# Kernel optimization log

Hardware: AMD Instinct MI355X
Metric: run time of the kernel (lower is better)

Reference implementation:

```python
import math
import jax, jax.numpy as jnp
import numpy as np

BATCH, DEPTH = 16, 12
N_NODES = 2 ** DEPTH - 1  # 4095, heap layout: children of i are 2i+1, 2i+2
IN_F, OUT_F, STATE_F = 512, 512, 256


def setup_inputs() -> dict:
    key = jax.random.key(0)
    ks = jax.random.split(key, 10)
    x_batch = jax.random.normal(ks[0], (BATCH, N_NODES, IN_F), dtype=jnp.float32)
    idx_batch = jnp.arange(BATCH, dtype=jnp.int32)
    W_in = jax.random.normal(ks[1], (IN_F, IN_F), dtype=jnp.float32) / math.sqrt(IN_F)
    b_in = jnp.zeros((IN_F,), dtype=jnp.float32)
    u1 = jax.random.uniform(ks[2], (STATE_F,), dtype=jnp.float32)
    u2 = jax.random.uniform(ks[3], (STATE_F,), dtype=jnp.float32)
    nu_log = jnp.log(-0.5 * jnp.log(u1 + 1e-6))
    theta_log = jnp.log(2.0 * math.pi * u2)
    lam_mod = jnp.exp(-jnp.exp(nu_log))
    gamma_log = jnp.log(jnp.sqrt(1.0 - jnp.square(lam_mod)))
    B_re = jax.random.normal(ks[4], (STATE_F, IN_F), dtype=jnp.float32) / math.sqrt(2 * IN_F)
    B_im = jax.random.normal(ks[5], (STATE_F, IN_F), dtype=jnp.float32) / math.sqrt(2 * IN_F)
    C_re = jax.random.normal(ks[6], (OUT_F, STATE_F), dtype=jnp.float32) / math.sqrt(STATE_F)
    C_im = jax.random.normal(ks[7], (OUT_F, STATE_F), dtype=jnp.float32) / math.sqrt(STATE_F)
    return dict(x_batch=x_batch, idx_batch=idx_batch, W_in=W_in, b_in=b_in,
                nu_log=nu_log, theta_log=theta_log, gamma_log=gamma_log,
                B_re=B_re, B_im=B_im, C_re=C_re, C_im=C_im)


def reference(x_batch, idx_batch, W_in, b_in, nu_log, theta_log, gamma_log,
              B_re, B_im, C_re, C_im):
    bsz, n_nodes, _ = x_batch.shape
    depth = int(round(math.log2(n_nodes + 1)))
    S = B_re.shape[0]

    # LRU constants (complex lambda kept as (re, im) pair)
    lam_mod = jnp.exp(-jnp.exp(nu_log))           # [S]
    th = jnp.exp(theta_log)
    lr, li = lam_mod * jnp.cos(th), lam_mod * jnp.sin(th)
    gamma = jnp.exp(gamma_log)                    # [S]

    proj = x_batch @ W_in.T + b_in                # [B, N, IN]
    # complex input term (proj is real): proj @ B^T
    in_re = jnp.einsum('bni,si->bns', proj, B_re) # [B, N, S]
    in_im = jnp.einsum('bni,si->bns', proj, B_im)

    h_re = jnp.zeros((bsz, n_nodes, S), dtype=proj.dtype)
    h_im = jnp.zeros((bsz, n_nodes, S), dtype=proj.dtype)

    # process levels bottom-up; level d nodes occupy [2^d-1, 2^{d+1}-1)
    for d in range(depth - 1, -1, -1):
        a, b = 2 ** d - 1, 2 ** (d + 1) - 1
        n = b - a
        if d == depth - 1:  # leaves: left/right = -1 -> zero child state
            cr = jnp.zeros((bsz, n, S), dtype=proj.dtype)
            ci = jnp.zeros((bsz, n, S), dtype=proj.dtype)
        else:
            # children of nodes [a, b) are the contiguous block [2a+1, 2b+1)
            cr = h_re[:, 2 * a + 1:2 * b + 1].reshape(bsz, n, 2, S).sum(axis=2)
            ci = h_im[:, 2 * a + 1:2 * b + 1].reshape(bsz, n, 2, S).sum(axis=2)
        hr = lr * cr - li * ci + gamma * in_re[:, a:b]
        hi = lr * ci + li * cr + gamma * in_im[:, a:b]
        h_re = h_re.at[:, a:b].set(hr)
        h_im = h_im.at[:, a:b].set(hi)

    # y = Re(h @ C^T), computed once on final states (same math as per-level scatter)
    outputs = jnp.einsum('bns,os->bno', h_re, C_re) - jnp.einsum('bns,os->bno', h_im, C_im)
    return outputs
```

## Files before the change

### kernel.cpp

```cpp
#include <hip/hip_runtime.h>


#define ROWS 65520
#define KDIM 512

typedef __attribute__((ext_vector_type(8))) short bf16x8;
typedef __attribute__((ext_vector_type(4))) float f32x4;

__device__ __forceinline__ unsigned short f2bf(float f) {
    unsigned int u = __float_as_uint(f);
    unsigned int r = (u + 0x7FFFu + ((u >> 16) & 1u)) >> 16;
    return (unsigned short)r;
}
__device__ __forceinline__ float b2f(unsigned short h) {
    return __uint_as_float(((unsigned int)h) << 16);
}
__device__ __forceinline__ float b2f_lo(unsigned int p) {
    return __uint_as_float(p << 16);
}
__device__ __forceinline__ float b2f_hi(unsigned int p) {
    return __uint_as_float(p & 0xFFFF0000u);
}

#define PC_BASE   1024
#define PB_BASE   2048
#define CVT_BASE  2176
#define CVT_BLKS  2048
#define PREP_GRID 4224
#define CVT_N4    8386560
#define CVT_STR   (CVT_BLKS * 256)

__global__ __launch_bounds__(256) void prep_all(const float* __restrict__ x,
                                                unsigned short* __restrict__ x16,
                                                const float* __restrict__ W,
                                                const float* __restrict__ Bre,
                                                const float* __restrict__ Bim,
                                                const float* __restrict__ gamma_log,
                                                unsigned short* __restrict__ M16,
                                                const float* __restrict__ bin,
                                                float* __restrict__ biasc,
                                                const float* __restrict__ Cre,
                                                const float* __restrict__ Cim,
                                                unsigned short* __restrict__ C16) {
    __shared__ float Bs[16][17];
    __shared__ float Ws[16][17];
    const int blk = blockIdx.x;
    const int t = threadIdx.x;

    if (blk < PC_BASE) {
        const int bx = blk & 31;
        const int by = blk >> 5;
        const int tx = t & 15;
        const int ty = t >> 4;
        const int j  = bx * 16 + tx;
        const int cc = by * 16 + ty;
        const float* Bsel = (cc < 256) ? (Bre + (size_t)cc * 512)
                                       : (Bim + (size_t)(cc - 256) * 512);
        float acc = 0.f;
        for (int kt = 0; kt < 512; kt += 16) {
            Bs[ty][tx] = Bsel[kt + tx];
            Ws[ty][tx] = W[(size_t)(kt + ty) * 512 + j];
            __syncthreads();
#pragma unroll
            for (int k = 0; k < 16; ++k) acc += Bs[ty][k] * Ws[k][tx];
            __syncthreads();
        }
        float g = expf(gamma_log[cc & 255]);
        M16[(size_t)cc * 512 + j] = f2bf(acc * g);
    } else if (blk < PB_BASE) {
        int idx = (blk - PC_BASE) * 256 + t;
        int o = idx >> 9;
        int s = idx & 511;
        float v = (s < 256) ? Cre[(size_t)o * 256 + s] : -Cim[(size_t)o * 256 + (s - 256)];
        C16[idx] = f2bf(v);
    } else if (blk < CVT_BASE) {
        const int c = (blk - PB_BASE) * 4 + (t >> 6);
        const int lane = t & 63;
        const float* Bsel = (c < 256) ? (Bre + (size_t)c * 512)
                                      : (Bim + (size_t)(c - 256) * 512);
        float acc = 0.f;
#pragma unroll
        for (int i = lane; i < 512; i += 64) acc += bin[i] * Bsel[i];
#pragma unroll
        for (int off = 32; off > 0; off >>= 1) acc += __shfl_down(acc, off, 64);
        if (lane == 0) biasc[c] = acc * expf(gamma_log[c & 255]);
    } else {
        const int i = (blk - CVT_BASE) * 256 + t;
        const float4* src = (const float4*)x;
        ushort4* dst = (ushort4*)x16;
        if (i < CVT_N4 - 15 * CVT_STR) {
            float4 v0  = src[i];
            float4 v1  = src[i +  1 * CVT_STR];
            float4 v2  = src[i +  2 * CVT_STR];
            float4 v3  = src[i +  3 * CVT_STR];
            float4 v4  = src[i +  4 * CVT_STR];
            float4 v5  = src[i +  5 * CVT_STR];
            float4 v6  = src[i +  6 * CVT_STR];
            float4 v7  = src[i +  7 * CVT_STR];
            float4 v8  = src[i +  8 * CVT_STR];
            float4 v9  = src[i +  9 * CVT_STR];
            float4 v10 = src[i + 10 * CVT_STR];
            float4 v11 = src[i + 11 * CVT_STR];
            float4 v12 = src[i + 12 * CVT_STR];
            float4 v13 = src[i + 13 * CVT_STR];
            float4 v14 = src[i + 14 * CVT_STR];
            float4 v15 = src[i + 15 * CVT_STR];
#define CVT1(K, V)                                                             \
            { ushort4 o; o.x = f2bf(V.x); o.y = f2bf(V.y);                     \
              o.z = f2bf(V.z); o.w = f2bf(V.w); dst[i + (K) * CVT_STR] = o; }
            CVT1(0, v0)  CVT1(1, v1)  CVT1(2, v2)  CVT1(3, v3)
            CVT1(4, v4)  CVT1(5, v5)  CVT1(6, v6)  CVT1(7, v7)
            CVT1(8, v8)  CVT1(9, v9)  CVT1(10, v10) CVT1(11, v11)
            CVT1(12, v12) CVT1(13, v13) CVT1(14, v14) CVT1(15, v15)
#undef CVT1
        } else {
#pragma unroll
            for (int k = 0; k < 16; ++k) {
                int idx = i + k * CVT_STR;
                if (idx < CVT_N4) {
                    float4 v = src[idx];
                    ushort4 o;
                    o.x = f2bf(v.x); o.y = f2bf(v.y); o.z = f2bf(v.z); o.w = f2bf(v.w);
                    dst[idx] = o;
                }
            }
        }
    }
}

template <bool OUT_BF16>
__global__ __launch_bounds__(256) void gemm_mfma(const unsigned short* __restrict__ A,
                                                 const unsigned short* __restrict__ Bm,
                                                 const float* __restrict__ bias,
                                                 void* __restrict__ Cout,
                                                 int Mrows) {
    __shared__ __align__(16) unsigned short As[2][128 * 32];
    __shared__ __align__(16) unsigned short Bs[2][128 * 32];
    const int t = threadIdx.x;
    const int lane = t & 63;
    const int w = t >> 6;
    const int wr = (w >> 1) * 64;
    const int wc = (w & 1) * 64;
    const int p = blockIdx.x;
    const int xcd = p & 7;
    const int q = p >> 3;
    const int colblk = q & 3;
    const int rg = q >> 2;
    const int col0 = colblk * 128;

    int arow[2], akoff[2], ldsoff[2];
    const unsigned short* gbB[2];
#pragma unroll
    for (int qq = 0; qq < 2; ++qq) {
        int c_   = qq * 256 + t;
        int row_ = c_ >> 2;
        int sl_  = c_ & 3;
        int kc_  = (sl_ - (row_ >> 1)) & 3;
        arow[qq]  = row_;
        akoff[qq] = kc_ * 8;
        ldsoff[qq] = c_ * 8;
        gbB[qq] = Bm + (size_t)(col0 + row_) * KDIM + kc_ * 8;
    }
    const unsigned short* gaB[2];

#define SET_TILE_A(ROW0)                                                       \
    do {                                                                       \
        _Pragma("unroll")                                                      \
        for (int qq = 0; qq < 2; ++qq) {                                       \
            int ar_ = (ROW0) + arow[qq]; if (ar_ >= Mrows) ar_ = Mrows - 1;    \
            gaB[qq] = A + (size_t)ar_ * KDIM + akoff[qq];                      \
        }                                                                      \
    } while (0)

#define STAGE(pb, KT)                                                          \
    do {                                                                       \
        _Pragma("unroll")                                                      \
        for (int qq = 0; qq < 2; ++qq) {                                       \
            __builtin_amdgcn_global_load_lds(                                  \
                (const __attribute__((address_space(1))) unsigned int*)(gaB[qq] + (KT)), \
                (__attribute__((address_space(3))) unsigned int*)(&As[pb][ldsoff[qq]]), \
                16, 0, 0);                                                     \
            __builtin_amdgcn_global_load_lds(                                  \
                (const __attribute__((address_space(1))) unsigned int*)(gbB[qq] + (KT)), \
                (__attribute__((address_space(3))) unsigned int*)(&Bs[pb][ldsoff[qq]]), \
                16, 0, 0);                                                     \
        }                                                                      \
    } while (0)

    f32x4 acc[4][4] = {};

    int rowblk = xcd * 64 + rg * 4;
    int row0 = rowblk * 128;
    int kt0 = (rowblk & 15) * 32;
    SET_TILE_A(row0);
    STAGE(0, kt0);
    __syncthreads();

    int cur = 0;
    for (int j = 0; j < 4; ++j) {
        for (int it = 0; it < 16; ++it) {
            if (it < 15) {
                STAGE(cur ^ 1, (kt0 + (it + 1) * 32) & 511);
            } else if (j < 3) {
                const int nrowblk = rowblk + 1;
                SET_TILE_A(nrowblk * 128);
                STAGE(cur ^ 1, (nrowblk & 15) * 32);
            }
            __builtin_amdgcn_s_setprio(1);
            {
                bf16x8 af[4], bfr[4];
#pragma unroll
                for (int i = 0; i < 4; ++i) {
                    int row = wr + i * 16 + (lane & 15);
                    int sa  = ((lane >> 4) + (row >> 1)) & 3;
                    af[i] = *(const bf16x8*)(&As[cur][row * 32 + sa * 8]);
                    int colr = wc + i * 16 + (lane & 15);
                    int sb  = ((lane >> 4) + (colr >> 1)) & 3;
                    bfr[i] = *(const bf16x8*)(&Bs[cur][colr * 32 + sb * 8]);
                }
#pragma unroll
                for (int i = 0; i < 4; ++i)
#pragma unroll
                    for (int jj = 0; jj < 4; ++jj)
                        acc[i][jj] = __builtin_amdgcn_mfma_f32_16x16x32_bf16(
                            af[i], bfr[jj], acc[i][jj], 0, 0, 0);
            }
            __builtin_amdgcn_s_setprio(0);
            __syncthreads();
            cur ^= 1;
        }

        const int cq = lane >> 4;
        const int cl = lane & 15;
#pragma unroll
        for (int i = 0; i < 4; ++i) {
#pragma unroll
            for (int jj = 0; jj < 4; ++jj) {
#pragma unroll
                for (int r = 0; r < 4; ++r) {
                    int grow = row0 + wr + i * 16 + cq * 4 + r;
                    int gcol = col0 + wc + jj * 16 + cl;
                    if (grow < Mrows) {
                        float v = acc[i][jj][r];
                        if (bias) v += bias[gcol];
                        if (OUT_BF16)
                            ((unsigned short*)Cout)[(size_t)grow * 512 + gcol] = f2bf(v);
                        else
                            ((float*)Cout)[(size_t)grow * 512 + gcol] = v;
                    }
                    acc[i][jj][r] = 0.f;
                }
            }
        }

        rowblk += 1;
        row0 = rowblk * 128;
        kt0 = (rowblk & 15) * 32;
    }
#undef STAGE
#undef SET_TILE_A
}

template <int E>
__global__ __launch_bounds__(256) void tree_up2(unsigned short* __restrict__ buf,
                                                const float* __restrict__ nu_log,
                                                const float* __restrict__ theta_log,
                                                int root_base, int nroots) {
    const int b = blockIdx.x;
    const int h = threadIdx.x >> 7;
    const int j2 = (threadIdx.x & 127) * 2;
    const int rr = blockIdx.y * 2 + h;
    if (rr >= nroots) return;
    const int rs = root_base + rr;
    constexpr int LEAVES = 1 << E;
    constexpr int NODES = LEAVES - 1;

    float lr0, li0, lr1, li1;
    { const float lam = expf(-expf(nu_log[j2]));     const float th = expf(theta_log[j2]);
      lr0 = lam * cosf(th); li0 = lam * sinf(th); }
    { const float lam = expf(-expf(nu_log[j2 + 1])); const float th = expf(theta_log[j2 + 1]);
      lr1 = lam * cosf(th); li1 = lam * sinf(th); }
    const size_t base = (size_t)b * 4095;

    unsigned int pr[LEAVES], pi[LEAVES];
    const int nbL = ((rs + 1) << E) - 1;
#pragma unroll
    for (int i = 0; i < LEAVES; ++i) {
        const size_t r = (base + nbL + i) * 512;
        pr[i] = *(const unsigned int*)(buf + r + j2);
        pi[i] = *(const unsigned int*)(buf + r + 256 + j2);
    }
    unsigned int qr[NODES], qi[NODES];
#pragma unroll
    for (int e = E - 1; e >= 0; --e) {
#pragma unroll
        for (int i = 0; i < (1 << e); ++i) {
            const int idx = LEAVES - (2 << e) + i;
            const size_t r = (base + (((rs + 1) << e) - 1) + i) * 512;
            qr[idx] = *(const unsigned int*)(buf + r + j2);
            qi[idx] = *(const unsigned int*)(buf + r + 256 + j2);
        }
    }
    __builtin_amdgcn_sched_barrier(0);

    float vr0[LEAVES], vi0[LEAVES], vr1[LEAVES], vi1[LEAVES];
#pragma unroll
    for (int i = 0; i < LEAVES; ++i) {
        vr0[i] = b2f_lo(pr[i]); vr1[i] = b2f_hi(pr[i]);
        vi0[i] = b2f_lo(pi[i]); vi1[i] = b2f_hi(pi[i]);
    }
#pragma unroll
    for (int e = E - 1; e >= 0; --e) {
#pragma unroll
        for (int i = 0; i < (1 << e); ++i) {
            const int idx = LEAVES - (2 << e) + i;
            const float cr0 = vr0[2 * i] + vr0[2 * i + 1];
            const float ci0 = vi0[2 * i] + vi0[2 * i + 1];
            const float cr1 = vr1[2 * i] + vr1[2 * i + 1];
            const float ci1 = vi1[2 * i] + vi1[2 * i + 1];
            const float hr0 = lr0 * cr0 - li0 * ci0 + b2f_lo(qr[idx]);
            const float hi0 = lr0 * ci0 + li0 * cr0 + b2f_lo(qi[idx]);
            const float hr1 = lr1 * cr1 - li1 * ci1 + b2f_hi(qr[idx]);
            const float hi1 = lr1 * ci1 + li1 * cr1 + b2f_hi(qi[idx]);
            const size_t r = (base + (((rs + 1) << e) - 1) + i) * 512;
            *(unsigned int*)(buf + r + j2) =
                (unsigned int)f2bf(hr0) | ((unsigned int)f2bf(hr1) << 16);
            *(unsigned int*)(buf + r + 256 + j2) =
                (unsigned int)f2bf(hi0) | ((unsigned int)f2bf(hi1) << 16);
            vr0[i] = hr0; vi0[i] = hi0; vr1[i] = hr1; vi1[i] = hi1;
        }
    }
}

extern "C" void kernel_launch(void* const* d_in, const int* in_sizes, int n_in,
                              void* d_out, int out_size, void* d_ws, size_t ws_size,
                              hipStream_t stream) {
    const float* x         = (const float*)d_in[0];
    const float* W_in      = (const float*)d_in[2];
    const float* b_in      = (const float*)d_in[3];
    const float* nu_log    = (const float*)d_in[4];
    const float* theta_log = (const float*)d_in[5];
    const float* gamma_log = (const float*)d_in[6];
    const float* B_re      = (const float*)d_in[7];
    const float* B_im      = (const float*)d_in[8];
    const float* C_re      = (const float*)d_in[9];
    const float* C_im      = (const float*)d_in[10];
    float* out = (float*)d_out;

    char* ws = (char*)d_ws;
    const size_t HB = (size_t)ROWS * 512 * 2;
    unsigned short* x16   = (unsigned short*)ws;
    unsigned short* hb16  = (unsigned short*)(ws + HB);
    unsigned short* M16   = (unsigned short*)(ws + 2 * HB);
    unsigned short* C16   = (unsigned short*)(ws + 2 * HB + 512 * 512 * 2);
    float*          biasc = (float*)(ws + 2 * HB + 2 * 512 * 512 * 2);

    prep_all<<<PREP_GRID, 256, 0, stream>>>(x, x16, W_in, B_re, B_im, gamma_log,
                                            M16, b_in, biasc, C_re, C_im, C16);

    gemm_mfma<true><<<512, 256, 0, stream>>>(x16, M16, biasc, hb16, ROWS);

    tree_up2<4><<<dim3(16, 64), 256, 0, stream>>>(hb16, nu_log, theta_log, 127, 128);
    tree_up2<4><<<dim3(16, 4),  256, 0, stream>>>(hb16, nu_log, theta_log, 7, 8);
    tree_up2<3><<<dim3(16, 1),  256, 0, stream>>>(hb16, nu_log, theta_log, 0, 1);

    gemm_mfma<false><<<512, 256, 0, stream>>>(hb16, C16, nullptr, out, ROWS);
}
```

Measured before the change: 413.4 us.

## Retile GEMM to 256x256 blocks with 8 waves and split-phase staging

Each GEMM block now computes a 256x256 output tile with 512 threads (8 waves), replacing the 128x128 tile of 4 waves that looped over four row blocks. The K step grows to 64 with an XOR swizzle in LDS. Loads for the next stage are spread across four sub-phases separated by explicit s_barrier and vmcnt waits. The aim is more data reuse per byte loaded and better overlap of global-to-LDS copies with MFMA work, at the cost of 128KB of LDS, a large accumulator array (register pressure), and more barriers.

Result: no change. 406.8 us (-1.6%).

```diff
diff --git a/kernel.cpp b/kernel.cpp
--- a/kernel.cpp
+++ b/kernel.cpp
@@ -129,136 +129,146 @@
 }
 
 template <bool OUT_BF16>
-__global__ __launch_bounds__(256) void gemm_mfma(const unsigned short* __restrict__ A,
-                                                 const unsigned short* __restrict__ Bm,
-                                                 const float* __restrict__ bias,
-                                                 void* __restrict__ Cout,
-                                                 int Mrows) {
-    __shared__ __align__(16) unsigned short As[2][128 * 32];
-    __shared__ __align__(16) unsigned short Bs[2][128 * 32];
+__global__ __launch_bounds__(512, 2) void gemm_mfma(const unsigned short* __restrict__ A,
+                                                    const unsigned short* __restrict__ Bm,
+                                                    const float* __restrict__ bias,
+                                                    void* __restrict__ Cout,
+                                                    int Mrows) {
+    __shared__ __align__(16) unsigned short As[2][16384];
+    __shared__ __align__(16) unsigned short Bs[2][16384];
     const int t = threadIdx.x;
     const int lane = t & 63;
-    const int w = t >> 6;
-    const int wr = (w >> 1) * 64;
-    const int wc = (w & 1) * 64;
-    const int p = blockIdx.x;
-    const int xcd = p & 7;
-    const int q = p >> 3;
-    const int colblk = q & 3;
-    const int rg = q >> 2;
-    const int col0 = colblk * 128;
-
-    int arow[2], akoff[2], ldsoff[2];
-    const unsigned short* gbB[2];
-#pragma unroll
-    for (int qq = 0; qq < 2; ++qq) {
-        int c_   = qq * 256 + t;
-        int row_ = c_ >> 2;
-        int sl_  = c_ & 3;
-        int kc_  = (sl_ - (row_ >> 1)) & 3;
-        arow[qq]  = row_;
-        akoff[qq] = kc_ * 8;
-        ldsoff[qq] = c_ * 8;
-        gbB[qq] = Bm + (size_t)(col0 + row_) * KDIM + kc_ * 8;
-    }
-    const unsigned short* gaB[2];
-
-#define SET_TILE_A(ROW0)                                                       \
+    const int wn = t >> 6;
+    const int bid = blockIdx.x;
+    const int xcd = bid & 7;
+    const int lid = bid >> 3;
+    const int rt = xcd * 32 + (lid >> 1);
+    const int ct = lid & 1;
+    const int row0 = rt * 256;
+    const int col0 = ct * 256;
+
+    const unsigned short* gA[2][2];
+    const unsigned short* gB[2][2];
+#pragma unroll
+    for (int h = 0; h < 2; ++h) {
+#pragma unroll
+        for (int q = 0; q < 2; ++q) {
+            int c2  = q * 512 + t;
+            int row = c2 >> 3;
+            int kc  = c2 & 7;
+            int lrow = h * 128 + row;
+            int kg  = kc ^ (lrow & 7);
+            int ar  = row0 + lrow; if (ar >= Mrows) ar = Mrows - 1;
+            gA[h][q] = A + (size_t)ar * KDIM + kg * 8;
+            gB[h][q] = Bm + (size_t)(col0 + lrow) * KDIM + kg * 8;
+        }
+    }
+
+#define STG_A(BUF, H, KT)                                                      \
     do {                                                                       \
         _Pragma("unroll")                                                      \
-        for (int qq = 0; qq < 2; ++qq) {                                       \
-            int ar_ = (ROW0) + arow[qq]; if (ar_ >= Mrows) ar_ = Mrows - 1;    \
-            gaB[qq] = A + (size_t)ar_ * KDIM + akoff[qq];                      \
-        }                                                                      \
+        for (int q = 0; q < 2; ++q)                                            \
+            __builtin_amdgcn_global_load_lds(                                  \
+                (const __attribute__((address_space(1))) unsigned int*)(gA[H][q] + (KT)), \
+                (__attribute__((address_space(3))) unsigned int*)(&As[BUF][(H) * 8192 + (q * 512 + t) * 8]), \
+                16, 0, 0);                                                     \
     } while (0)
-
-#define STAGE(pb, KT)                                                          \
+#define STG_B(BUF, H, KT)                                                      \
     do {                                                                       \
         _Pragma("unroll")                                                      \
-        for (int qq = 0; qq < 2; ++qq) {                                       \
+        for (int q = 0; q < 2; ++q)                                            \
             __builtin_amdgcn_global_load_lds(                                  \
-                (const __attribute__((address_space(1))) unsigned int*)(gaB[qq] + (KT)), \
-                (__attribute__((address_space(3))) unsigned int*)(&As[pb][ldsoff[qq]]), \
+                (const __attribute__((address_space(1))) unsigned int*)(gB[H][q] + (KT)), \
+                (__attribute__((address_space(3))) unsigned int*)(&Bs[BUF][(H) * 8192 + (q * 512 + t) * 8]), \
                 16, 0, 0);                                                     \
-            __builtin_amdgcn_global_load_lds(                                  \
-                (const __attribute__((address_space(1))) unsigned int*)(gbB[qq] + (KT)), \
-                (__attribute__((address_space(3))) unsigned int*)(&Bs[pb][ldsoff[qq]]), \
-                16, 0, 0);                                                     \
-        }                                                                      \
     } while (0)
-
-    f32x4 acc[4][4] = {};
-
-    int rowblk = xcd * 64 + rg * 4;
-    int row0 = rowblk * 128;
-    int kt0 = (rowblk & 15) * 32;
-    SET_TILE_A(row0);
-    STAGE(0, kt0);
-    __syncthreads();
-
-    int cur = 0;
-    for (int j = 0; j < 4; ++j) {
-        for (int it = 0; it < 16; ++it) {
-            if (it < 15) {
-                STAGE(cur ^ 1, (kt0 + (it + 1) * 32) & 511);
-            } else if (j < 3) {
-                const int nrowblk = rowblk + 1;
-                SET_TILE_A(nrowblk * 128);
-                STAGE(cur ^ 1, (nrowblk & 15) * 32);
-            }
+#define BARRIER() asm volatile("s_barrier" ::: "memory")
+
+    f32x4 acc[16][2] = {};
+
+#define KTOF(S) ((((rt & 7) + (S)) & 7) * 64)
+
+    {
+        const int kt = KTOF(0);
+        STG_B(0, 0, kt); STG_B(0, 1, kt); STG_A(0, 0, kt); STG_A(0, 1, kt);
+    }
+
+    for (int s = 0; s < 8; ++s) {
+        const int cur = s & 1;
+        const int nkt = KTOF(s + 1);
+        asm volatile("s_waitcnt vmcnt(2)" ::: "memory");
+        BARRIER();
+#pragma unroll
+        for (int p = 0; p < 4; ++p) {
+            bf16x8 af[4][2], bfr[2][2];
+#pragma unroll
+            for (int i = 0; i < 4; ++i) {
+                int row = p * 64 + i * 16 + (lane & 15);
+#pragma unroll
+                for (int kk = 0; kk < 2; ++kk) {
+                    int kca = (kk * 4 + (lane >> 4)) ^ (row & 7);
+                    af[i][kk] = *(const bf16x8*)(&As[cur][row * 64 + kca * 8]);
+                }
+            }
+#pragma unroll
+            for (int j = 0; j < 2; ++j) {
+                int colr = wn * 32 + j * 16 + (lane & 15);
+#pragma unroll
+                for (int kk = 0; kk < 2; ++kk) {
+                    int kcb = (kk * 4 + (lane >> 4)) ^ (colr & 7);
+                    bfr[j][kk] = *(const bf16x8*)(&Bs[cur][colr * 64 + kcb * 8]);
+                }
+            }
+            if (s < 7) {
+                if (p == 0)      STG_B(cur ^ 1, 0, nkt);
+                else if (p == 1) STG_B(cur ^ 1, 1, nkt);
+                else if (p == 2) STG_A(cur ^ 1, 0, nkt);
+                else             STG_A(cur ^ 1, 1, nkt);
+            }
+            BARRIER();
             __builtin_amdgcn_s_setprio(1);
-            {
-                bf16x8 af[4], bfr[4];
-#pragma unroll
-                for (int i = 0; i < 4; ++i) {
-                    int row = wr + i * 16 + (lane & 15);
-                    int sa  = ((lane >> 4) + (row >> 1)) & 3;
-                    af[i] = *(const bf16x8*)(&As[cur][row * 32 + sa * 8]);
-                    int colr = wc + i * 16 + (lane & 15);
-                    int sb  = ((lane >> 4) + (colr >> 1)) & 3;
-                    bfr[i] = *(const bf16x8*)(&Bs[cur][colr * 32 + sb * 8]);
+#pragma unroll
+            for (int i = 0; i < 4; ++i)
+#pragma unroll
+                for (int j = 0; j < 2; ++j)
+#pragma unroll
+                    for (int kk = 0; kk < 2; ++kk)
+                        acc[p * 4 + i][j] = __builtin_amdgcn_mfma_f32_16x16x32_bf16(
+                            af[i][kk], bfr[j][kk], acc[p * 4 + i][j], 0, 0, 0);
+            __builtin_amdgcn_s_setprio(0);
+            if (p == 1) {
+                if (s < 7) asm volatile("s_waitcnt vmcnt(4)" ::: "memory");
+                else       asm volatile("s_waitcnt vmcnt(0)" ::: "memory");
+            }
+            BARRIER();
+        }
+    }
+#undef KTOF
+#undef BARRIER
+#undef STG_B
+#undef STG_A
+
+    const int cq = lane >> 4;
+    const int cl = lane & 15;
+#pragma unroll
+    for (int I = 0; I < 16; ++I) {
+#pragma unroll
+        for (int j = 0; j < 2; ++j) {
+#pragma unroll
+            for (int r = 0; r < 4; ++r) {
+                int grow = row0 + I * 16 + cq * 4 + r;
+                int gcol = col0 + wn * 32 + j * 16 + cl;
+                if (grow < Mrows) {
+                    float v = acc[I][j][r];
+                    if (bias) v += bias[gcol];
+                    if (OUT_BF16)
+                        ((unsigned short*)Cout)[(size_t)grow * 512 + gcol] = f2bf(v);
+                    else
+                        ((float*)Cout)[(size_t)grow * 512 + gcol] = v;
                 }
-#pragma unroll
-                for (int i = 0; i < 4; ++i)
-#pragma unroll
-                    for (int jj = 0; jj < 4; ++jj)
-                        acc[i][jj] = __builtin_amdgcn_mfma_f32_16x16x32_bf16(
-                            af[i], bfr[jj], acc[i][jj], 0, 0, 0);
-            }
-            __builtin_amdgcn_s_setprio(0);
-            __syncthreads();
-            cur ^= 1;
-        }
-
-        const int cq = lane >> 4;
-        const int cl = lane & 15;
-#pragma unroll
-        for (int i = 0; i < 4; ++i) {
-#pragma unroll
-            for (int jj = 0; jj < 4; ++jj) {
-#pragma unroll
-                for (int r = 0; r < 4; ++r) {
-                    int grow = row0 + wr + i * 16 + cq * 4 + r;
-                    int gcol = col0 + wc + jj * 16 + cl;
-                    if (grow < Mrows) {
-                        float v = acc[i][jj][r];
-                        if (bias) v += bias[gcol];
-                        if (OUT_BF16)
-                            ((unsigned short*)Cout)[(size_t)grow * 512 + gcol] = f2bf(v);
-                        else
-                            ((float*)Cout)[(size_t)grow * 512 + gcol] = v;
-                    }
-                    acc[i][jj][r] = 0.f;
-                }
-            }
-        }
-
-        rowblk += 1;
-        row0 = rowblk * 128;
-        kt0 = (rowblk & 15) * 32;
-    }
-#undef STAGE
-#undef SET_TILE_A
+            }
+        }
+    }
 }
 
 template <int E>
@@ -358,11 +368,11 @@
     prep_all<<<PREP_GRID, 256, 0, stream>>>(x, x16, W_in, B_re, B_im, gamma_log,
                                             M16, b_in, biasc, C_re, C_im, C16);
 
-    gemm_mfma<true><<<512, 256, 0, stream>>>(x16, M16, biasc, hb16, ROWS);
+    gemm_mfma<true><<<512, 512, 0, stream>>>(x16, M16, biasc, hb16, ROWS);
 
     tree_up2<4><<<dim3(16, 64), 256, 0, stream>>>(hb16, nu_log, theta_log, 127, 128);
     tree_up2<4><<<dim3(16, 4),  256, 0, stream>>>(hb16, nu_log, theta_log, 7, 8);
     tree_up2<3><<<dim3(16, 1),  256, 0, stream>>>(hb16, nu_log, theta_log, 0, 1);
 
-    gemm_mfma<false><<<512, 256, 0, stream>>>(hb16, C16, nullptr, out, ROWS);
-}
+    gemm_mfma<false><<<512, 512, 0, stream>>>(hb16, C16, nullptr, out, ROWS);
+}
```

## Launch one GEMM tile per block with 2048 blocks instead of persistent loop

Applied to the files above, without the earlier changes.

The GEMM kernel no longer loops over four row tiles per block. Each block now computes a single 128x128 tile, and the grid grows from 512 to 2048 blocks, with launch bounds asking for 4 blocks per CU. This is meant to raise occupancy and let the hardware overlap one block's epilogue stores with other blocks' compute, instead of serialising them inside a persistent block. A sched_barrier is also added to the fp32-to-bf16 conversion loop to keep all loads issued ahead of the converts, at the cost of some scheduler freedom and possible register pressure.

Measured after the change: 373.5 us. 9.6% less time.

```diff
diff --git a/kernel.cpp b/kernel.cpp
--- a/kernel.cpp
+++ b/kernel.cpp
@@ -105,6 +105,7 @@
             float4 v13 = src[i + 13 * CVT_STR];
             float4 v14 = src[i + 14 * CVT_STR];
             float4 v15 = src[i + 15 * CVT_STR];
+            __builtin_amdgcn_sched_barrier(0);
 #define CVT1(K, V)                                                             \
             { ushort4 o; o.x = f2bf(V.x); o.y = f2bf(V.y);                     \
               o.z = f2bf(V.z); o.w = f2bf(V.w); dst[i + (K) * CVT_STR] = o; }
@@ -129,11 +130,11 @@
 }
 
 template <bool OUT_BF16>
-__global__ __launch_bounds__(256) void gemm_mfma(const unsigned short* __restrict__ A,
-                                                 const unsigned short* __restrict__ Bm,
-                                                 const float* __restrict__ bias,
-                                                 void* __restrict__ Cout,
-                                                 int Mrows) {
+__global__ __launch_bounds__(256, 4) void gemm_mfma(const unsigned short* __restrict__ A,
+                                                    const unsigned short* __restrict__ Bm,
+                                                    const float* __restrict__ bias,
+                                                    void* __restrict__ Cout,
+                                                    int Mrows) {
     __shared__ __align__(16) unsigned short As[2][128 * 32];
     __shared__ __align__(16) unsigned short Bs[2][128 * 32];
     const int t = threadIdx.x;
@@ -141,36 +142,29 @@
     const int w = t >> 6;
     const int wr = (w >> 1) * 64;
     const int wc = (w & 1) * 64;
-    const int p = blockIdx.x;
-    const int xcd = p & 7;
-    const int q = p >> 3;
-    const int colblk = q & 3;
-    const int rg = q >> 2;
+    const int bid = blockIdx.x;
+    const int xcd = bid & 7;
+    const int lid = bid >> 3;
+    const int rowblk = xcd * 64 + (lid >> 2);
+    const int colblk = lid & 3;
+    const int row0 = rowblk * 128;
     const int col0 = colblk * 128;
-
-    int arow[2], akoff[2], ldsoff[2];
+    const int kt0  = (rowblk & 15) * 32;
+
+    const unsigned short* gaB[2];
     const unsigned short* gbB[2];
+    int ldsoff[2];
 #pragma unroll
     for (int qq = 0; qq < 2; ++qq) {
         int c_   = qq * 256 + t;
         int row_ = c_ >> 2;
         int sl_  = c_ & 3;
         int kc_  = (sl_ - (row_ >> 1)) & 3;
-        arow[qq]  = row_;
-        akoff[qq] = kc_ * 8;
+        int ar_  = row0 + row_; if (ar_ >= Mrows) ar_ = Mrows - 1;
+        gaB[qq] = A + (size_t)ar_ * KDIM + kc_ * 8;
+        gbB[qq] = Bm + (size_t)(col0 + row_) * KDIM + kc_ * 8;
         ldsoff[qq] = c_ * 8;
-        gbB[qq] = Bm + (size_t)(col0 + row_) * KDIM + kc_ * 8;
-    }
-    const unsigned short* gaB[2];
-
-#define SET_TILE_A(ROW0)                                                       \
-    do {                                                                       \
-        _Pragma("unroll")                                                      \
-        for (int qq = 0; qq < 2; ++qq) {                                       \
-            int ar_ = (ROW0) + arow[qq]; if (ar_ >= Mrows) ar_ = Mrows - 1;    \
-            gaB[qq] = A + (size_t)ar_ * KDIM + akoff[qq];                      \
-        }                                                                      \
-    } while (0)
+    }
 
 #define STAGE(pb, KT)                                                          \
     do {                                                                       \
@@ -189,76 +183,58 @@
 
     f32x4 acc[4][4] = {};
 
-    int rowblk = xcd * 64 + rg * 4;
-    int row0 = rowblk * 128;
-    int kt0 = (rowblk & 15) * 32;
-    SET_TILE_A(row0);
     STAGE(0, kt0);
     __syncthreads();
 
     int cur = 0;
-    for (int j = 0; j < 4; ++j) {
-        for (int it = 0; it < 16; ++it) {
-            if (it < 15) {
-                STAGE(cur ^ 1, (kt0 + (it + 1) * 32) & 511);
-            } else if (j < 3) {
-                const int nrowblk = rowblk + 1;
-                SET_TILE_A(nrowblk * 128);
-                STAGE(cur ^ 1, (nrowblk & 15) * 32);
+    for (int it = 0; it < 16; ++it) {
+        if (it < 15) STAGE(cur ^ 1, (kt0 + (it + 1) * 32) & 511);
+        __builtin_amdgcn_s_setprio(1);
+        {
+            bf16x8 af[4], bfr[4];
+#pragma unroll
+            for (int i = 0; i < 4; ++i) {
+                int row = wr + i * 16 + (lane & 15);
+                int sa  = ((lane >> 4) + (row >> 1)) & 3;
+                af[i] = *(const bf16x8*)(&As[cur][row * 32 + sa * 8]);
+                int colr = wc + i * 16 + (lane & 15);
+                int sb  = ((lane >> 4) + (colr >> 1)) & 3;
+                bfr[i] = *(const bf16x8*)(&Bs[cur][colr * 32 + sb * 8]);
             }
-            __builtin_amdgcn_s_setprio(1);
-            {
-                bf16x8 af[4], bfr[4];
-#pragma unroll
-                for (int i = 0; i < 4; ++i) {
-                    int row = wr + i * 16 + (lane & 15);
-                    int sa  = ((lane >> 4) + (row >> 1)) & 3;
-                    af[i] = *(const bf16x8*)(&As[cur][row * 32 + sa * 8]);
-                    int colr = wc + i * 16 + (lane & 15);
-                    int sb  = ((lane >> 4) + (colr >> 1)) & 3;
-                    bfr[i] = *(const bf16x8*)(&Bs[cur][colr * 32 + sb * 8]);
-                }
-#pragma unroll
-                for (int i = 0; i < 4; ++i)
-#pragma unroll
-                    for (int jj = 0; jj < 4; ++jj)
-                        acc[i][jj] = __builtin_amdgcn_mfma_f32_16x16x32_bf16(
-                            af[i], bfr[jj], acc[i][jj], 0, 0, 0);
-            }
-            __builtin_amdgcn_s_setprio(0);
-            __syncthreads();
-            cur ^= 1;
-        }
-
-        const int cq = lane >> 4;
-        const int cl = lane & 15;
-#pragma unroll
-        for (int i = 0; i < 4; ++i) {
-#pragma unroll
-            for (int jj = 0; jj < 4; ++jj) {
-#pragma unroll
-                for (int r = 0; r < 4; ++r) {
-                    int grow = row0 + wr + i * 16 + cq * 4 + r;
-                    int gcol = col0 + wc + jj * 16 + cl;
-                    if (grow < Mrows) {
-                        float v = acc[i][jj][r];
-                        if (bias) v += bias[gcol];
-                        if (OUT_BF16)
-                            ((unsigned short*)Cout)[(size_t)grow * 512 + gcol] = f2bf(v);
-                        else
-                            ((float*)Cout)[(size_t)grow * 512 + gcol] = v;
-                    }
-                    acc[i][jj][r] = 0.f;
+#pragma unroll
+            for (int i = 0; i < 4; ++i)
+#pragma unroll
+                for (int jj = 0; jj < 4; ++jj)
+                    acc[i][jj] = __builtin_amdgcn_mfma_f32_16x16x32_bf16(
+                        af[i], bfr[jj], acc[i][jj], 0, 0, 0);
+        }
+        __builtin_amdgcn_s_setprio(0);
+        __syncthreads();
+        cur ^= 1;
+    }
+#undef STAGE
+
+    const int cq = lane >> 4;
+    const int cl = lane & 15;
+#pragma unroll
+    for (int i = 0; i < 4; ++i) {
+#pragma unroll
+        for (int jj = 0; jj < 4; ++jj) {
+#pragma unroll
+            for (int r = 0; r < 4; ++r) {
+                int grow = row0 + wr + i * 16 + cq * 4 + r;
+                int gcol = col0 + wc + jj * 16 + cl;
+                if (grow < Mrows) {
+                    float v = acc[i][jj][r];
+                    if (bias) v += bias[gcol];
+                    if (OUT_BF16)
+                        ((unsigned short*)Cout)[(size_t)grow * 512 + gcol] = f2bf(v);
+                    else
+                        ((float*)Cout)[(size_t)grow * 512 + gcol] = v;
                 }
             }
         }
-
-        rowblk += 1;
-        row0 = rowblk * 128;
-        kt0 = (rowblk & 15) * 32;
-    }
-#undef STAGE
-#undef SET_TILE_A
+    }
 }
 
 template <int E>
@@ -358,11 +334,11 @@
     prep_all<<<PREP_GRID, 256, 0, stream>>>(x, x16, W_in, B_re, B_im, gamma_log,
                                             M16, b_in, biasc, C_re, C_im, C16);
 
-    gemm_mfma<true><<<512, 256, 0, stream>>>(x16, M16, biasc, hb16, ROWS);
+    gemm_mfma<true><<<2048, 256, 0, stream>>>(x16, M16, biasc, hb16, ROWS);
 
     tree_up2<4><<<dim3(16, 64), 256, 0, stream>>>(hb16, nu_log, theta_log, 127, 128);
     tree_up2<4><<<dim3(16, 4),  256, 0, stream>>>(hb16, nu_log, theta_log, 7, 8);
     tree_up2<3><<<dim3(16, 1),  256, 0, stream>>>(hb16, nu_log, theta_log, 0, 1);
 
-    gemm_mfma<false><<<512, 256, 0, stream>>>(hb16, C16, nullptr, out, ROWS);
-}
+    gemm_mfma<false><<<2048, 256, 0, stream>>>(hb16, C16, nullptr, out, ROWS);
+}
```
